# Kernel optimization log

Measured on AMD Instinct MI355X. Metric: run time of the kernel, lower is better.

Reference implementation:

```python
import jax, jax.numpy as jnp
import numpy as np

D_MODEL = 512
N_HEADS = 8
D_K = D_MODEL // N_HEADS


def setup_inputs() -> dict:
    key = jax.random.key(0)
    ks = jax.random.split(key, 9)
    s = 1.0 / np.sqrt(D_MODEL)
    x = jax.random.normal(ks[0], (2, 4096, D_MODEL), dtype=jnp.float32)
    def lin(kw, kb):
        W = jax.random.uniform(kw, (D_MODEL, D_MODEL), jnp.float32, -s, s)
        b = jax.random.uniform(kb, (D_MODEL,), jnp.float32, -s, s)
        return W, b
    Wq, bq = lin(ks[1], ks[2])
    Wk, bk = lin(ks[3], ks[4])
    Wv, bv = lin(ks[5], ks[6])
    Wo, bo = lin(ks[7], ks[8])
    return {"x": x, "Wq": Wq, "bq": bq, "Wk": Wk, "bk": bk,
            "Wv": Wv, "bv": bv, "Wo": Wo, "bo": bo}


def reference(x, Wq, bq, Wk, bk, Wv, bv, Wo, bo):
    B, T, C = x.shape
    # project and split heads: [B, H, T, d_k]
    def heads(W, b):
        return (x @ W.T + b).reshape(B, T, N_HEADS, D_K).transpose(0, 2, 1, 3)
    q = heads(Wq, bq)
    k = heads(Wk, bk)
    v = heads(Wv, bv)
    scores = jnp.einsum('bhqd,bhkd->bhqk', q, k) / np.sqrt(D_K).astype(jnp.float32)
    attn = jax.nn.softmax(scores, axis=-1)  # dropout p=0 (eval)
    out = jnp.einsum('bhqk,bhkd->bhqd', attn, v)
    out = out.transpose(0, 2, 1, 3).reshape(B, T, C)
    return out @ Wo.T + bo
```

## Files before the change

### kernel.cpp

```cpp
#include <hip/hip_runtime.h>

typedef _Float16 f16x8 __attribute__((ext_vector_type(8)));
typedef _Float16 f16x4 __attribute__((ext_vector_type(4)));
typedef float f32x4 __attribute__((ext_vector_type(4)));

__global__ void cvt_all(const float* __restrict__ x,
                        const float* __restrict__ Wq, const float* __restrict__ Wk,
                        const float* __restrict__ Wv, const float* __restrict__ Wo,
                        _Float16* __restrict__ xf, _Float16* __restrict__ wf) {
  int g = blockIdx.x * blockDim.x + threadIdx.x;
  const float* src;
  _Float16* dst;
  if (g < 524288) {
    src = x + (size_t)g * 8;
    dst = xf + (size_t)g * 8;
  } else {
    int g2 = g - 524288;
    int z = g2 >> 15, off = g2 & 32767;
    const float* W = (z == 0) ? Wq : (z == 1) ? Wk : (z == 2) ? Wv : Wo;
    src = W + (size_t)off * 8;
    dst = wf + (size_t)z * 262144 + (size_t)off * 8;
  }
  f32x4 a = *(const f32x4*)src;
  f32x4 b = *(const f32x4*)(src + 4);
  f16x8 o;
  o[0] = (_Float16)a[0]; o[1] = (_Float16)a[1];
  o[2] = (_Float16)a[2]; o[3] = (_Float16)a[3];
  o[4] = (_Float16)b[0]; o[5] = (_Float16)b[1];
  o[6] = (_Float16)b[2]; o[7] = (_Float16)b[3];
  *(f16x8*)dst = o;
}

__global__ __launch_bounds__(256, 2)
void qkv_gemm(const _Float16* __restrict__ X, const _Float16* __restrict__ Wf,
              const float* __restrict__ bq, const float* __restrict__ bk,
              const float* __restrict__ bv, _Float16* __restrict__ dst3) {
  __shared__ __align__(16) _Float16 As[128][72];
  __shared__ __align__(16) _Float16 Bs[128][72];
  const int z = blockIdx.z;
  const _Float16* Wz = Wf + (size_t)z * 262144;
  const float* bias = (z == 0) ? bq : (z == 1 ? bk : bv);
  _Float16* dst = dst3 + (size_t)z * 4194304;
  const float scale = (z == 0) ? 0.18033688011112042f : 1.0f;

  const int t = threadIdx.x;
  const int lane = t & 63, wave = t >> 6;
  const int quad = lane >> 4, col = lane & 15;
  const int wm = (wave & 1) * 64, wn = (wave >> 1) * 64;
  const int m0 = blockIdx.x * 128, n0 = blockIdx.y * 128;

  f32x4 acc[4][4] = {};

  for (int k0 = 0; k0 < 512; k0 += 64) {
    __syncthreads();
#pragma unroll
    for (int i = 0; i < 4; i++) {
      int flat = i * 2048 + t * 8;
      int r = flat >> 6, c = flat & 63;
      *(f16x8*)&As[r][c] = *(const f16x8*)&X[(size_t)(m0 + r) * 512 + k0 + c];
      *(f16x8*)&Bs[r][c] = *(const f16x8*)&Wz[(size_t)(n0 + r) * 512 + k0 + c];
    }
    __syncthreads();
#pragma unroll
    for (int ks = 0; ks < 2; ks++) {
      f16x8 a[4], b[4];
#pragma unroll
      for (int i = 0; i < 4; i++) {
        a[i] = *(const f16x8*)&As[wm + i * 16 + col][ks * 32 + quad * 8];
        b[i] = *(const f16x8*)&Bs[wn + i * 16 + col][ks * 32 + quad * 8];
      }
#pragma unroll
      for (int mi = 0; mi < 4; mi++)
#pragma unroll
        for (int ni = 0; ni < 4; ni++)
          acc[mi][ni] = __builtin_amdgcn_mfma_f32_16x16x32_f16(a[mi], b[ni], acc[mi][ni], 0, 0, 0);
    }
  }

#pragma unroll
  for (int ni = 0; ni < 4; ni++) {
    int n = n0 + wn + ni * 16 + col;
    float bv_ = bias[n];
    int h = n >> 6, d = n & 63;
#pragma unroll
    for (int mi = 0; mi < 4; mi++) {
#pragma unroll
      for (int r = 0; r < 4; r++) {
        int m = m0 + wm + mi * 16 + quad * 4 + r;
        int b = m >> 12, tt = m & 4095;
        float v = (acc[mi][ni][r] + bv_) * scale;
        dst[((size_t)(b * 8 + h) * 4096 + tt) * 64 + d] = (_Float16)v;
      }
    }
  }
}

__global__ __launch_bounds__(256, 2)
void attn_kernel(const _Float16* __restrict__ Q, const _Float16* __restrict__ K,
                 const _Float16* __restrict__ V, _Float16* __restrict__ O) {
  __shared__ __align__(16) _Float16 Ks[2][128][72];
  __shared__ __align__(16) _Float16 Vt[2][64][136];

  const int t = threadIdx.x;
  const int lane = t & 63, wave = t >> 6;
  const int quad = lane >> 4, col = lane & 15;
  const int bh = blockIdx.y;
  const int q0 = blockIdx.x * 128;
  const _Float16* Qb = Q + (size_t)bh * 4096 * 64;
  const _Float16* Kbh = K + (size_t)bh * 4096 * 64;
  const _Float16* Vbh = V + (size_t)bh * 4096 * 64;

  const int sr = (t * 8) >> 6, sc = (t * 8) & 63;
  const int vd = t & 63, kb0 = (t >> 6) * 8;

  f16x8 qf[2][2];
#pragma unroll
  for (int mt = 0; mt < 2; mt++)
#pragma unroll
    for (int ks = 0; ks < 2; ks++)
      qf[mt][ks] = *(const f16x8*)&Qb[(size_t)(q0 + wave * 32 + mt * 16 + col) * 64 +
                                      ks * 32 + quad * 8];

  f16x8 kreg[4], vreg[4];
  {
    const _Float16* Kb = Kbh;
    const _Float16* Vb = Vbh;
#pragma unroll
    for (int i = 0; i < 4; i++)
      kreg[i] = *(const f16x8*)&Kb[(size_t)(sr + 32 * i) * 64 + sc];
#pragma unroll
    for (int it = 0; it < 4; it++) {
      int kb = it * 32 + kb0;
      f16x8 vv;
#pragma unroll
      for (int u = 0; u < 8; u++) vv[u] = Vb[(size_t)(kb + u) * 64 + vd];
      vreg[it] = vv;
    }
  }
#pragma unroll
  for (int i = 0; i < 4; i++)
    *(f16x8*)&Ks[0][sr + 32 * i][sc] = kreg[i];
#pragma unroll
  for (int it = 0; it < 4; it++)
    *(f16x8*)&Vt[0][vd][it * 32 + kb0] = vreg[it];
  __syncthreads();

  f32x4 o_acc[2][4] = {};
  float l_acc[2] = {0.f, 0.f};

  for (int j = 0; j < 32; j++) {
    const int buf = j & 1;
    if (j + 1 < 32) {
      const _Float16* Kb = Kbh + (size_t)(j + 1) * 128 * 64;
      const _Float16* Vb = Vbh + (size_t)(j + 1) * 128 * 64;
#pragma unroll
      for (int i = 0; i < 4; i++)
        kreg[i] = *(const f16x8*)&Kb[(size_t)(sr + 32 * i) * 64 + sc];
#pragma unroll
      for (int it = 0; it < 4; it++) {
        int kb = it * 32 + kb0;
        f16x8 vv;
#pragma unroll
        for (int u = 0; u < 8; u++) vv[u] = Vb[(size_t)(kb + u) * 64 + vd];
        vreg[it] = vv;
      }
    }

    f32x4 s[2][8];
#pragma unroll
    for (int mt = 0; mt < 2; mt++)
#pragma unroll
      for (int nt = 0; nt < 8; nt++) s[mt][nt] = (f32x4){0.f, 0.f, 0.f, 0.f};
#pragma unroll
    for (int ks = 0; ks < 2; ks++) {
#pragma unroll
      for (int nt = 0; nt < 8; nt++) {
        f16x8 kf = *(const f16x8*)&Ks[buf][nt * 16 + col][ks * 32 + quad * 8];
#pragma unroll
        for (int mt = 0; mt < 2; mt++)
          s[mt][nt] = __builtin_amdgcn_mfma_f32_16x16x32_f16(kf, qf[mt][ks], s[mt][nt], 0, 0, 0);
      }
    }

    f16x4 pf[2][8];
#pragma unroll
    for (int mt = 0; mt < 2; mt++) {
#pragma unroll
      for (int nt = 0; nt < 8; nt++) {
#pragma unroll
        for (int r = 0; r < 4; r++) {
          float p = exp2f(s[mt][nt][r]);
          l_acc[mt] += p;
          pf[mt][nt][r] = (_Float16)p;
        }
      }
    }

#pragma unroll
    for (int nt = 0; nt < 8; nt++) {
#pragma unroll
      for (int dt = 0; dt < 4; dt++) {
        f16x4 vf = *(const f16x4*)&Vt[buf][dt * 16 + col][nt * 16 + quad * 4];
#pragma unroll
        for (int mt = 0; mt < 2; mt++)
          o_acc[mt][dt] = __builtin_amdgcn_mfma_f32_16x16x16f16(vf, pf[mt][nt], o_acc[mt][dt], 0, 0, 0);
      }
    }

    if (j + 1 < 32) {
      const int nb = buf ^ 1;
#pragma unroll
      for (int i = 0; i < 4; i++)
        *(f16x8*)&Ks[nb][sr + 32 * i][sc] = kreg[i];
#pragma unroll
      for (int it = 0; it < 4; it++)
        *(f16x8*)&Vt[nb][vd][it * 32 + kb0] = vreg[it];
      __syncthreads();
    }
  }

#pragma unroll
  for (int mt = 0; mt < 2; mt++) {
    l_acc[mt] += __shfl_xor(l_acc[mt], 16);
    l_acc[mt] += __shfl_xor(l_acc[mt], 32);
  }

  const int b = bh >> 3, h = bh & 7;
#pragma unroll
  for (int mt = 0; mt < 2; mt++) {
    int row = q0 + wave * 32 + mt * 16 + col;
    float inv = 1.0f / l_acc[mt];
#pragma unroll
    for (int dt = 0; dt < 4; dt++) {
      f16x4 ov;
#pragma unroll
      for (int r = 0; r < 4; r++) ov[r] = (_Float16)(o_acc[mt][dt][r] * inv);
      *(f16x4*)&O[((size_t)(b * 4096 + row)) * 512 + h * 64 + dt * 16 + quad * 4] = ov;
    }
  }
}

__global__ __launch_bounds__(256, 2)
void out_gemm(const _Float16* __restrict__ X, const _Float16* __restrict__ Wo,
              const float* __restrict__ bias, float* __restrict__ out) {
  __shared__ __align__(16) _Float16 As[128][72];
  __shared__ __align__(16) _Float16 Bs[128][72];
  const int t = threadIdx.x;
  const int lane = t & 63, wave = t >> 6;
  const int quad = lane >> 4, col = lane & 15;
  const int wm = (wave & 1) * 64, wn = (wave >> 1) * 64;
  const int m0 = blockIdx.x * 128, n0 = blockIdx.y * 128;

  f32x4 acc[4][4] = {};

  for (int k0 = 0; k0 < 512; k0 += 64) {
    __syncthreads();
#pragma unroll
    for (int i = 0; i < 4; i++) {
      int flat = i * 2048 + t * 8;
      int r = flat >> 6, c = flat & 63;
      *(f16x8*)&As[r][c] = *(const f16x8*)&X[(size_t)(m0 + r) * 512 + k0 + c];
      *(f16x8*)&Bs[r][c] = *(const f16x8*)&Wo[(size_t)(n0 + r) * 512 + k0 + c];
    }
    __syncthreads();
#pragma unroll
    for (int ks = 0; ks < 2; ks++) {
      f16x8 a[4], b[4];
#pragma unroll
      for (int i = 0; i < 4; i++) {
        a[i] = *(const f16x8*)&As[wm + i * 16 + col][ks * 32 + quad * 8];
        b[i] = *(const f16x8*)&Bs[wn + i * 16 + col][ks * 32 + quad * 8];
      }
#pragma unroll
      for (int mi = 0; mi < 4; mi++)
#pragma unroll
        for (int ni = 0; ni < 4; ni++)
          acc[mi][ni] = __builtin_amdgcn_mfma_f32_16x16x32_f16(a[mi], b[ni], acc[mi][ni], 0, 0, 0);
    }
  }

#pragma unroll
  for (int ni = 0; ni < 4; ni++) {
    int n = n0 + wn + ni * 16 + col;
    float bv_ = bias[n];
#pragma unroll
    for (int mi = 0; mi < 4; mi++) {
#pragma unroll
      for (int r = 0; r < 4; r++) {
        int m = m0 + wm + mi * 16 + quad * 4 + r;
        out[(size_t)m * 512 + n] = acc[mi][ni][r] + bv_;
      }
    }
  }
}

extern "C" void kernel_launch(void* const* d_in, const int* in_sizes, int n_in,
                              void* d_out, int out_size, void* d_ws, size_t ws_size,
                              hipStream_t stream) {
  const float* x  = (const float*)d_in[0];
  const float* Wq = (const float*)d_in[1];
  const float* bq = (const float*)d_in[2];
  const float* Wk = (const float*)d_in[3];
  const float* bk = (const float*)d_in[4];
  const float* Wv = (const float*)d_in[5];
  const float* bv = (const float*)d_in[6];
  const float* Wo = (const float*)d_in[7];
  const float* bo = (const float*)d_in[8];

  char* ws = (char*)d_ws;
  _Float16* xf  = (_Float16*)(ws);
  _Float16* wf  = (_Float16*)(ws + (8u << 20));
  _Float16* qkv = (_Float16*)(ws + (10u << 20));
  _Float16* ao  = (_Float16*)(ws);

  cvt_all<<<2560, 256, 0, stream>>>(x, Wq, Wk, Wv, Wo, xf, wf);

  qkv_gemm<<<dim3(64, 4, 3), 256, 0, stream>>>(xf, wf, bq, bk, bv, qkv);

  attn_kernel<<<dim3(32, 16), 256, 0, stream>>>(qkv, qkv + 4194304,
                                                qkv + 2 * 4194304, ao);

  out_gemm<<<dim3(64, 4), 256, 0, stream>>>(ao, wf + 3 * 262144, bo,
                                            (float*)d_out);
}
```

Before: 226.5 us.

## Store V transposed from projection GEMM and compute row sums via MFMA

The QKV projection epilogue now writes V in a [bh][d][t] transposed layout with vectorized 4-wide stores, so the attention kernel can load V tiles with 16-byte global loads instead of eight scalar strided loads per vector. The Vt shared buffer padding changes to 132. The softmax denominator is now accumulated with an MFMA against a ones vector instead of scalar adds plus cross-lane shuffles. The score MFMAs are split so the first k-step starts from a zero accumulator. This trades a little extra MFMA work for fewer VALU ops and cheaper V loads, and the transposed projection stores may be less coalesced.

```diff
diff --git a/kernel.cpp b/kernel.cpp
--- a/kernel.cpp
+++ b/kernel.cpp
@@ -77,19 +77,37 @@
     }
   }
 
-#pragma unroll
-  for (int ni = 0; ni < 4; ni++) {
-    int n = n0 + wn + ni * 16 + col;
-    float bv_ = bias[n];
-    int h = n >> 6, d = n & 63;
-#pragma unroll
-    for (int mi = 0; mi < 4; mi++) {
-#pragma unroll
-      for (int r = 0; r < 4; r++) {
-        int m = m0 + wm + mi * 16 + quad * 4 + r;
+  if (z != 2) {
+#pragma unroll
+    for (int ni = 0; ni < 4; ni++) {
+      int n = n0 + wn + ni * 16 + col;
+      float bv_ = bias[n];
+      int h = n >> 6, d = n & 63;
+#pragma unroll
+      for (int mi = 0; mi < 4; mi++) {
+#pragma unroll
+        for (int r = 0; r < 4; r++) {
+          int m = m0 + wm + mi * 16 + quad * 4 + r;
+          int b = m >> 12, tt = m & 4095;
+          float v = (acc[mi][ni][r] + bv_) * scale;
+          dst[((size_t)(b * 8 + h) * 4096 + tt) * 64 + d] = (_Float16)v;
+        }
+      }
+    }
+  } else {
+#pragma unroll
+    for (int ni = 0; ni < 4; ni++) {
+      int n = n0 + wn + ni * 16 + col;
+      float bv_ = bias[n];
+      int h = n >> 6, d = n & 63;
+#pragma unroll
+      for (int mi = 0; mi < 4; mi++) {
+        int m = m0 + wm + mi * 16 + quad * 4;
         int b = m >> 12, tt = m & 4095;
-        float v = (acc[mi][ni][r] + bv_) * scale;
-        dst[((size_t)(b * 8 + h) * 4096 + tt) * 64 + d] = (_Float16)v;
+        f16x4 ov;
+#pragma unroll
+        for (int r = 0; r < 4; r++) ov[r] = (_Float16)(acc[mi][ni][r] + bv_);
+        *(f16x4*)&dst[((size_t)((b * 8 + h) * 64 + d)) * 4096 + tt] = ov;
       }
     }
   }
@@ -99,7 +117,7 @@
 void attn_kernel(const _Float16* __restrict__ Q, const _Float16* __restrict__ K,
                  const _Float16* __restrict__ V, _Float16* __restrict__ O) {
   __shared__ __align__(16) _Float16 Ks[2][128][72];
-  __shared__ __align__(16) _Float16 Vt[2][64][136];
+  __shared__ __align__(16) _Float16 Vt[2][64][132];
 
   const int t = threadIdx.x;
   const int lane = t & 63, wave = t >> 6;
@@ -108,10 +126,10 @@
   const int q0 = blockIdx.x * 128;
   const _Float16* Qb = Q + (size_t)bh * 4096 * 64;
   const _Float16* Kbh = K + (size_t)bh * 4096 * 64;
-  const _Float16* Vbh = V + (size_t)bh * 4096 * 64;
+  const _Float16* Vg = V + (size_t)bh * 64 * 4096;
 
   const int sr = (t * 8) >> 6, sc = (t * 8) & 63;
-  const int vd = t & 63, kb0 = (t >> 6) * 8;
+  const int vrow = t >> 4, vcol = (t & 15) * 8;
 
   f16x8 qf[2][2];
 #pragma unroll
@@ -121,80 +139,77 @@
       qf[mt][ks] = *(const f16x8*)&Qb[(size_t)(q0 + wave * 32 + mt * 16 + col) * 64 +
                                       ks * 32 + quad * 8];
 
+  f16x4 ones4;
+#pragma unroll
+  for (int i = 0; i < 4; i++) ones4[i] = (_Float16)1.0f;
+  const f32x4 fz = {0.f, 0.f, 0.f, 0.f};
+
   f16x8 kreg[4], vreg[4];
-  {
-    const _Float16* Kb = Kbh;
-    const _Float16* Vb = Vbh;
-#pragma unroll
-    for (int i = 0; i < 4; i++)
-      kreg[i] = *(const f16x8*)&Kb[(size_t)(sr + 32 * i) * 64 + sc];
-#pragma unroll
-    for (int it = 0; it < 4; it++) {
-      int kb = it * 32 + kb0;
-      f16x8 vv;
-#pragma unroll
-      for (int u = 0; u < 8; u++) vv[u] = Vb[(size_t)(kb + u) * 64 + vd];
-      vreg[it] = vv;
-    }
-  }
+#pragma unroll
+  for (int i = 0; i < 4; i++)
+    kreg[i] = *(const f16x8*)&Kbh[(size_t)(sr + 32 * i) * 64 + sc];
+#pragma unroll
+  for (int it = 0; it < 4; it++)
+    vreg[it] = *(const f16x8*)&Vg[(size_t)(it * 16 + vrow) * 4096 + vcol];
 #pragma unroll
   for (int i = 0; i < 4; i++)
     *(f16x8*)&Ks[0][sr + 32 * i][sc] = kreg[i];
 #pragma unroll
-  for (int it = 0; it < 4; it++)
-    *(f16x8*)&Vt[0][vd][it * 32 + kb0] = vreg[it];
+  for (int it = 0; it < 4; it++) {
+    f16x4 lo, hi;
+#pragma unroll
+    for (int u = 0; u < 4; u++) { lo[u] = vreg[it][u]; hi[u] = vreg[it][u + 4]; }
+    *(f16x4*)&Vt[0][it * 16 + vrow][vcol] = lo;
+    *(f16x4*)&Vt[0][it * 16 + vrow][vcol + 4] = hi;
+  }
   __syncthreads();
 
   f32x4 o_acc[2][4] = {};
-  float l_acc[2] = {0.f, 0.f};
+  f32x4 l4[2] = {};
 
   for (int j = 0; j < 32; j++) {
     const int buf = j & 1;
     if (j + 1 < 32) {
       const _Float16* Kb = Kbh + (size_t)(j + 1) * 128 * 64;
-      const _Float16* Vb = Vbh + (size_t)(j + 1) * 128 * 64;
 #pragma unroll
       for (int i = 0; i < 4; i++)
         kreg[i] = *(const f16x8*)&Kb[(size_t)(sr + 32 * i) * 64 + sc];
 #pragma unroll
-      for (int it = 0; it < 4; it++) {
-        int kb = it * 32 + kb0;
-        f16x8 vv;
-#pragma unroll
-        for (int u = 0; u < 8; u++) vv[u] = Vb[(size_t)(kb + u) * 64 + vd];
-        vreg[it] = vv;
-      }
+      for (int it = 0; it < 4; it++)
+        vreg[it] = *(const f16x8*)&Vg[(size_t)(it * 16 + vrow) * 4096 +
+                                      (j + 1) * 128 + vcol];
     }
 
     f32x4 s[2][8];
 #pragma unroll
+    for (int nt = 0; nt < 8; nt++) {
+      f16x8 kf = *(const f16x8*)&Ks[buf][nt * 16 + col][quad * 8];
+#pragma unroll
+      for (int mt = 0; mt < 2; mt++)
+        s[mt][nt] = __builtin_amdgcn_mfma_f32_16x16x32_f16(kf, qf[mt][0], fz, 0, 0, 0);
+    }
+#pragma unroll
+    for (int nt = 0; nt < 8; nt++) {
+      f16x8 kf = *(const f16x8*)&Ks[buf][nt * 16 + col][32 + quad * 8];
+#pragma unroll
+      for (int mt = 0; mt < 2; mt++)
+        s[mt][nt] = __builtin_amdgcn_mfma_f32_16x16x32_f16(kf, qf[mt][1], s[mt][nt], 0, 0, 0);
+    }
+
+    f16x4 pf[2][8];
+#pragma unroll
     for (int mt = 0; mt < 2; mt++)
 #pragma unroll
-      for (int nt = 0; nt < 8; nt++) s[mt][nt] = (f32x4){0.f, 0.f, 0.f, 0.f};
-#pragma unroll
-    for (int ks = 0; ks < 2; ks++) {
-#pragma unroll
-      for (int nt = 0; nt < 8; nt++) {
-        f16x8 kf = *(const f16x8*)&Ks[buf][nt * 16 + col][ks * 32 + quad * 8];
-#pragma unroll
-        for (int mt = 0; mt < 2; mt++)
-          s[mt][nt] = __builtin_amdgcn_mfma_f32_16x16x32_f16(kf, qf[mt][ks], s[mt][nt], 0, 0, 0);
-      }
-    }
-
-    f16x4 pf[2][8];
-#pragma unroll
-    for (int mt = 0; mt < 2; mt++) {
-#pragma unroll
-      for (int nt = 0; nt < 8; nt++) {
-#pragma unroll
-        for (int r = 0; r < 4; r++) {
-          float p = exp2f(s[mt][nt][r]);
-          l_acc[mt] += p;
-          pf[mt][nt][r] = (_Float16)p;
-        }
-      }
-    }
+      for (int nt = 0; nt < 8; nt++)
+#pragma unroll
+        for (int r = 0; r < 4; r++)
+          pf[mt][nt][r] = (_Float16)exp2f(s[mt][nt][r]);
+
+#pragma unroll
+    for (int mt = 0; mt < 2; mt++)
+#pragma unroll
+      for (int nt = 0; nt < 8; nt++)
+        l4[mt] = __builtin_amdgcn_mfma_f32_16x16x16f16(ones4, pf[mt][nt], l4[mt], 0, 0, 0);
 
 #pragma unroll
     for (int nt = 0; nt < 8; nt++) {
@@ -213,23 +228,22 @@
       for (int i = 0; i < 4; i++)
         *(f16x8*)&Ks[nb][sr + 32 * i][sc] = kreg[i];
 #pragma unroll
-      for (int it = 0; it < 4; it++)
-        *(f16x8*)&Vt[nb][vd][it * 32 + kb0] = vreg[it];
+      for (int it = 0; it < 4; it++) {
+        f16x4 lo, hi;
+#pragma unroll
+        for (int u = 0; u < 4; u++) { lo[u] = vreg[it][u]; hi[u] = vreg[it][u + 4]; }
+        *(f16x4*)&Vt[nb][it * 16 + vrow][vcol] = lo;
+        *(f16x4*)&Vt[nb][it * 16 + vrow][vcol + 4] = hi;
+      }
       __syncthreads();
     }
-  }
-
-#pragma unroll
-  for (int mt = 0; mt < 2; mt++) {
-    l_acc[mt] += __shfl_xor(l_acc[mt], 16);
-    l_acc[mt] += __shfl_xor(l_acc[mt], 32);
   }
 
   const int b = bh >> 3, h = bh & 7;
 #pragma unroll
   for (int mt = 0; mt < 2; mt++) {
     int row = q0 + wave * 32 + mt * 16 + col;
-    float inv = 1.0f / l_acc[mt];
+    float inv = 1.0f / l4[mt][0];
 #pragma unroll
     for (int dt = 0; dt < 4; dt++) {
       f16x4 ov;
```

Measured after the change: 225.3 us. About the same (-0.6%).
